# Kernel tuning notes

Hardware: AMD Instinct MI355X
Metric: run time of the kernel (lower is better)

Reference implementation:

```python
import jax, jax.numpy as jnp
import numpy as np

N = 100_000   # nodes
E = 3_200_000 # directed edges (avg degree 32)
D = 256       # feature dim (in_channels)
K = 2         # k of k-MIS


def _propagate_min(min_rank, row, col, n, k):
    # k iterations of scatter_min along edges (row -> col), keeping current value
    for _ in range(k):
        neigh = jax.ops.segment_min(min_rank[row], col, num_segments=n)
        min_rank = jnp.minimum(min_rank, neigh)
    return min_rank


def maximal_k_independent_set(row, col, rank, n, k):
    # Luby-style greedy k-MIS: repeatedly add nodes whose rank is minimal in their
    # k-hop in-neighbourhood, then mark (cover) the k-hop neighbourhood of the MIS.
    def dilate(mask):
        for _ in range(k):
            neigh = jax.ops.segment_max(mask[row].astype(jnp.int32), col, num_segments=n)
            mask = mask | (neigh > 0)
        return mask

    def cond(state):
        _, mask, _ = state
        return ~jnp.all(mask)

    def body(state):
        mis, mask, min_rank = state
        min_rank = _propagate_min(min_rank, row, col, n, k)
        mis = mis | (rank == min_rank)
        mask = dilate(mis)
        min_rank = jnp.where(mask, n, rank)  # covered nodes get rank 'infinity' (= n)
        return mis, mask, min_rank

    z = jnp.zeros((n,), dtype=bool)
    mis, _, _ = jax.lax.while_loop(cond, body, (z, z, rank))
    return mis


def cluster_k_mis(mis, row, col, rank, n, k):
    # min_rank = n everywhere except MIS nodes get their rank; propagate min k hops;
    # cluster id = index of the unique MIS rank each node ends up attached to.
    min_rank = jnp.where(mis, rank, n)
    min_rank = _propagate_min(min_rank, row, col, n, k)
    _, clusters = jnp.unique(min_rank, return_inverse=True)
    return clusters.reshape(-1).astype(jnp.int32)


def setup_inputs():
    key = jax.random.key(0)
    k1, k2, k3 = jax.random.split(key, 3)
    x = jax.random.normal(k1, (N, D), dtype=jnp.float32)
    edge_index = jax.random.randint(k2, (2, E), 0, N, dtype=jnp.int32)
    edge_attr = jax.random.normal(k3, (E,), dtype=jnp.float32)
    return {"x": x, "edge_index": edge_index, "edge_attr": edge_attr}


def reference(x, edge_index, edge_attr):
    n = x.shape[0]
    row, col = edge_index[0], edge_index[1]
    # scorer=None -> score = arange(n); greedy ordering of arange -> rank = arange(n)
    rank = jnp.arange(n, dtype=jnp.int32)

    mis = maximal_k_independent_set(row, col, rank, n, K)
    cluster = cluster_k_mis(mis, row, col, rank, n, K)
    c = int(mis.sum())  # number of clusters (MIS size)

    # --- pooled adjacency: coalesce duplicate (cluster[row], cluster[col]) with sum ---
    cl_np = np.asarray(cluster).astype(np.int64)
    r = cl_np[np.asarray(row)]
    cc = cl_np[np.asarray(col)]
    keys = r * np.int64(c) + cc
    uniq, inv = np.unique(keys, return_inverse=True)
    val = jax.ops.segment_sum(edge_attr, jnp.asarray(inv.astype(np.int32)),
                              num_segments=int(uniq.shape[0]))
    new_row = (uniq // c).astype(np.int32)
    new_col = (uniq % c).astype(np.int32)
    keep = np.nonzero(new_row != new_col)[0]  # remove_self_loops=True
    pooled_edge_index = jnp.stack([jnp.asarray(new_row[keep]), jnp.asarray(new_col[keep])])
    pooled_edge_attr = val[jnp.asarray(keep)]

    # --- pooled node features: reduce_x='sum' (adaptive=False, so no score scaling) ---
    x_pooled = jax.ops.segment_sum(x, cluster, num_segments=c)
    return x_pooled, pooled_edge_index, pooled_edge_attr
```

## Files before the change

### kernel.cpp

```cpp
#include <hip/hip_runtime.h>
#include <cmath>
#include <cstdint>

#define NT 256
#define EG0 1024
#define EG1 256
#define MAX_ROUND 16
#define SCAN_T 32
#define SCAN_IPB (NT*SCAN_T)
#define SENT 0x80000000u


__device__ __forceinline__ int block_append(int* cursor, bool pred, int* s_w){
  int wid  = threadIdx.x >> 6;
  int lane = threadIdx.x & 63;
  unsigned long long m = __ballot(pred);
  int cnt = __popcll(m);
  if(lane==0) s_w[wid]=cnt;
  __syncthreads();
  if(threadIdx.x==0){
    int t0=s_w[0], t1=s_w[1], t2=s_w[2], t3=s_w[3];
    int tot=t0+t1+t2+t3;
    int base = tot ? atomicAdd(cursor, tot) : 0;
    s_w[0]=base; s_w[1]=base+t0; s_w[2]=base+t0+t1; s_w[3]=base+t0+t1+t2;
  }
  __syncthreads();
  int pos = s_w[wid] + __popcll(m & ((1ull<<lane)-1ull));
  __syncthreads();
  return pos;
}


__global__ void k_init(int* a, int* b, int n){
  int v = blockIdx.x*NT + threadIdx.x;
  if(v<n){ a[v]=v; b[v]=v; }
}

__global__ void k_fill_dense(float* dense, long M){
  long stride = (long)gridDim.x*NT;
  for(long i = (long)blockIdx.x*NT + threadIdx.x; i<M; i+=stride)
    ((unsigned int*)dense)[i] = SENT;
}


__global__ void k_hop0(int* b, const int* __restrict__ row,
                       const int* __restrict__ col, int E){
  int stride = gridDim.x*NT;
  for(int e = blockIdx.x*NT + threadIdx.x; e<E; e+=stride){
    int s = row[e];
    if(s < b[col[e]]) atomicMin(&b[col[e]], s);
  }
}

__global__ void k_hop0f(int* a, const int* b, const int* __restrict__ row,
                        const int* __restrict__ col, int n, int E){
  int stride = gridDim.x*NT;
  int total = n + E;
  for(int i = blockIdx.x*NT + threadIdx.x; i<total; i+=stride){
    if(i<n){
      if(b[i] < a[i]) atomicMin(&a[i], b[i]);
    } else {
      int e = i-n;
      int s = b[row[e]];
      if(s < a[col[e]]) atomicMin(&a[col[e]], s);
    }
  }
}

__global__ void k_dil0(const int* a, int* d2, int* cover, const int* __restrict__ row,
                       const int* __restrict__ col, int E, int ep){
  int stride = gridDim.x*NT;
  for(int e = blockIdx.x*NT + threadIdx.x; e<E; e+=stride){
    int r = row[e];
    if(a[r]==r){
      int cc = col[e];
      d2[r]=ep;  cover[r]=1;
      d2[cc]=ep; cover[cc]=1;
    }
  }
}

__global__ void k_dil20(const int* a, const int* d2, int* cover, const int* __restrict__ row,
                        const int* __restrict__ col, int E, int ep){
  int stride = gridDim.x*NT;
  for(int e = blockIdx.x*NT + threadIdx.x; e<E; e+=stride){
    int r = row[e];
    if((d2[r]==ep || a[r]==r) && !cover[col[e]]) cover[col[e]]=1;
  }
}

__global__ void k_fincomp0(int* a, int* b, int* mis, int* cover, int n,
                           const int* __restrict__ row, const int* __restrict__ col, int E,
                           int2* Ld, int* lcnt1, int* U1, int* rcnt0){
  __shared__ int s_w[4];
  long nth = (long)gridDim.x*NT;
  for(long base = (long)blockIdx.x*NT; base < n; base += nth){
    int v = (int)base + threadIdx.x;
    bool unc = false;
    if(v<n){
      int nw = (a[v]==v);
      if(nw){ mis[v]=1; if(!cover[v]) cover[v]=1; }
      int cov = cover[v] | nw;
      int val = cov ? n : v;
      a[v]=val; b[v]=val;
      unc = !cov;
    }
    int pos = block_append(rcnt0, unc, s_w);
    if(unc) U1[pos]=v;
  }
  for(long base = (long)blockIdx.x*NT; base < E; base += nth){
    int e = (int)base + threadIdx.x;
    bool keep=false; int2 ed;
    if(e<E){
      ed = make_int2(row[e], col[e]);
      keep = (!cover[ed.x]) || (!cover[ed.y]);
    }
    int pos = block_append(lcnt1, keep, s_w);
    if(keep) Ld[pos]=ed;
  }
}


__global__ void k_hop1(int* b, const int* a, const int2* L, const int* pE,
                       const int* gate){
  if(*gate==0) return;
  int E = *pE;
  int stride = gridDim.x*NT;
  for(int e = blockIdx.x*NT + threadIdx.x; e<E; e+=stride){
    int2 ed = L[e];
    int s = a[ed.x];
    if(s < b[ed.y]) atomicMin(&b[ed.y], s);
  }
}

__global__ void k_hop1f(int* a, const int* b, const int2* L, const int* pE,
                        const int* U, const int* pU, const int* gate){
  if(*gate==0) return;
  int E = *pE, un = *pU;
  int total = un + E;
  int stride = gridDim.x*NT;
  for(int i = blockIdx.x*NT + threadIdx.x; i<total; i+=stride){
    if(i<un){
      int u = U[i];
      if(b[u] < a[u]) atomicMin(&a[u], b[u]);
    } else {
      int2 ed = L[i-un];
      int s = b[ed.x];
      if(s < a[ed.y]) atomicMin(&a[ed.y], s);
    }
  }
}

__global__ void k_dil11(const int* a, int* d2, int* cover, int* mis, const int2* L,
                        const int* pE, const int* U, const int* pU, const int* gate, int ep){
  if(*gate==0) return;
  int E = *pE, un = *pU;
  int total = un + E;
  int stride = gridDim.x*NT;
  for(int i = blockIdx.x*NT + threadIdx.x; i<total; i+=stride){
    if(i<un){
      int u = U[i];
      if(a[u]==u){ mis[u]=1; cover[u]=1; d2[u]=ep; }
    } else {
      int2 ed = L[i-un];
      if(a[ed.x]==ed.x){ d2[ed.x]=ep; cover[ed.x]=1; d2[ed.y]=ep; cover[ed.y]=1; }
    }
  }
}

__global__ void k_dil21(const int* a, const int* d2, int* cover, const int2* L,
                        const int* pE, const int* gate, int ep){
  if(*gate==0) return;
  int E = *pE;
  int stride = gridDim.x*NT;
  for(int e = blockIdx.x*NT + threadIdx.x; e<E; e+=stride){
    int2 ed = L[e];
    if((d2[ed.x]==ep || a[ed.x]==ed.x) && !cover[ed.y]) cover[ed.y]=1;
  }
}

__global__ void k_fincomp1(int* a, int* b, const int* cover, int n,
                           const int2* Ls, const int* pE, int2* Ld, int* lcntD,
                           const int* Us, const int* pU, int* Ud, int* rcntD,
                           const int* gate){
  if(*gate==0) return;
  __shared__ int s_w[4];
  int E = *pE, un = *pU;
  long nth = (long)gridDim.x*NT;
  for(long base = (long)blockIdx.x*NT; base < un; base += nth){
    int i = (int)base + threadIdx.x;
    bool unc=false; int u=0;
    if(i<un){ u = Us[i]; unc = !cover[u]; }
    int pos = block_append(rcntD, unc, s_w);
    if(unc) Ud[pos]=u;
  }
  for(long base = (long)blockIdx.x*NT; base < E; base += nth){
    int e = (int)base + threadIdx.x;
    bool keep=false; int2 ed;
    if(e<E){
      ed = Ls[e];
      int vx = cover[ed.x] ? n : ed.x;  a[ed.x]=vx; b[ed.x]=vx;
      int vy = cover[ed.y] ? n : ed.y;  a[ed.y]=vy; b[ed.y]=vy;
      keep = (!cover[ed.x]) || (!cover[ed.y]);
    }
    int pos = block_append(lcntD, keep, s_w);
    if(keep) Ld[pos]=ed;
  }
}


__global__ void k_cluster_init(const int* mis, int* a, int* b, int n){
  int v = blockIdx.x*NT + threadIdx.x;
  if(v<n){ int m = mis[v] ? v : n; a[v]=m; b[v]=m; }
}

__global__ void k_chop1(int* b, const int* a, const int* __restrict__ row,
                        const int* __restrict__ col, int n, int E){
  int stride = gridDim.x*NT;
  for(int e = blockIdx.x*NT + threadIdx.x; e<E; e+=stride){
    int s = a[row[e]];
    if(s < n && s < b[col[e]]) atomicMin(&b[col[e]], s);
  }
}

__global__ void k_chop2f(int* a, const int* b, const int* __restrict__ row,
                         const int* __restrict__ col, int n, int E){
  int stride = gridDim.x*NT;
  int total = n + E;
  for(int i = blockIdx.x*NT + threadIdx.x; i<total; i+=stride){
    if(i<n){
      if(b[i] < a[i]) atomicMin(&a[i], b[i]);
    } else {
      int e = i-n;
      int s = b[row[e]];
      if(s < n && s < a[col[e]]) atomicMin(&a[col[e]], s);
    }
  }
}

__global__ void k_mark(const int* mr, const int* mis, int* present, int* cmis, int n){
  int v = blockIdx.x*NT + threadIdx.x;
  int m = 0;
  if(v<n){
    int r = mr[v];
    if(r<n) present[r]=1;
    m = mis[v];
  }
  __shared__ int sh[NT];
  sh[threadIdx.x]=m; __syncthreads();
  for(int off=NT/2; off>0; off>>=1){
    if(threadIdx.x<off) sh[threadIdx.x]+=sh[threadIdx.x+off];
    __syncthreads();
  }
  if(threadIdx.x==0 && sh[0]) atomicAdd(cmis, sh[0]);
}


__global__ void k_scan1(const int* A, int M, int* bsum){
  int t = threadIdx.x;
  long base = (long)blockIdx.x*SCAN_IPB + (long)t*SCAN_T;
  int s = 0;
  #pragma unroll
  for(int j=0;j<SCAN_T;j++){ long i=base+j; if(i<M) s += A[i]; }
  __shared__ int sh[NT];
  sh[t]=s; __syncthreads();
  for(int off=NT/2; off>0; off>>=1){ if(t<off) sh[t]+=sh[t+off]; __syncthreads(); }
  if(t==0) bsum[blockIdx.x]=sh[0];
}

__global__ void k_scan2(const int* bsum, int* bscan, int B, int* totalOut){
  __shared__ int sh[NT];
  int t = threadIdx.x;
  int carry = 0;
  for(int base=0; base<B; base+=NT){
    int i = base+t;
    int v = (i<B) ? bsum[i] : 0;
    sh[t]=v; __syncthreads();
    for(int off=1; off<NT; off<<=1){
      int x=0; if(t>=off) x=sh[t-off];
      __syncthreads();
      sh[t]+=x; __syncthreads();
    }
    int incl = sh[t];
    if(i<B) bscan[i] = carry + incl - v;
    carry += sh[NT-1];
    __syncthreads();
  }
  if(t==0 && totalOut) *totalOut = carry;
}

__global__ void k_scan3(const int* A, int M, const int* bscan, int* pref){
  int t = threadIdx.x;
  long base = (long)blockIdx.x*SCAN_IPB + (long)t*SCAN_T;
  int s = 0;
  #pragma unroll
  for(int j=0;j<SCAN_T;j++){ long i=base+j; if(i<M) s += A[i]; }
  __shared__ int sh[NT];
  sh[t]=s; __syncthreads();
  for(int off=1; off<NT; off<<=1){
    int x=0; if(t>=off) x=sh[t-off];
    __syncthreads();
    sh[t]+=x; __syncthreads();
  }
  int run = bscan[blockIdx.x] + (sh[t]-s);
  for(int j=0;j<SCAN_T;j++){
    long i=base+j;
    if(i<M){ pref[i]=run; run += A[i]; }
  }
}


__global__ void k_assign(const int* mr, const int* pref, int* cl, int* ccount, int n){
  int v = blockIdx.x*NT + threadIdx.x;
  if(v<n){
    int r = mr[v];
    int cid = (r<n) ? pref[r] : 0;
    cl[v]=cid;
    atomicAdd(&ccount[cid],1);
  }
}

__global__ void k_scatter_nodes(const int* cl, const int* cstart, int* cursor, int* nodeList, int n){
  int v = blockIdx.x*NT + threadIdx.x;
  if(v<n){
    int cid = cl[v];
    int pos = cstart[cid] + atomicAdd(&cursor[cid],1);
    nodeList[pos]=v;
  }
}

__global__ void k_pool_x(const float* __restrict__ x, const int* nodeList, const int* cstart,
                         const int* ccount, const int* scal, float* out, long out_size){
  int c = scal[0], U = scal[1];
  int t = threadIdx.x;
  for(int cid=blockIdx.x; cid<c; cid+=gridDim.x){
    float s0=0.f, s1=0.f, s2=0.f, s3=0.f;
    if(cid<U){
      int st = cstart[cid], cn = ccount[cid];
      int i=0;
      for(; i+3<cn; i+=4){
        int n0=nodeList[st+i], n1=nodeList[st+i+1], n2=nodeList[st+i+2], n3=nodeList[st+i+3];
        s0 += x[(size_t)n0*256 + t];
        s1 += x[(size_t)n1*256 + t];
        s2 += x[(size_t)n2*256 + t];
        s3 += x[(size_t)n3*256 + t];
      }
      for(; i<cn; i++) s0 += x[(size_t)nodeList[st+i]*256 + t];
      s0 += s1+s2+s3;
    }
    long idx = (long)cid*256 + t;
    if(idx < out_size) out[idx]=s0;
  }
}

__global__ void k_edge_pool(const int* __restrict__ row, const int* __restrict__ col,
                            const float* __restrict__ attr, const int* cl,
                            const int* scal, float* dense, int E, long CMsq){
  int c = scal[0];
  int stride = gridDim.x*NT;
  for(int e = blockIdx.x*NT + threadIdx.x; e<E; e+=stride){
    long key = (long)cl[row[e]]*c + cl[col[e]];
    if(key < CMsq){
      unsafeAtomicAdd(&dense[key], attr[e]);
    }
  }
}

__device__ __forceinline__ int cellp(const float* dense, long i){
  return __float_as_uint(dense[i]) != SENT;
}

__global__ void k_cscan1(const float* dense, const int* scal, int* bsum, long CMsq){
  int c = scal[0];
  long M = (long)c*c; if(M>CMsq) M=CMsq;
  int t = threadIdx.x;
  long base = (long)blockIdx.x*SCAN_IPB + (long)t*SCAN_T;
  int s = 0;
  if(base < M && c > 0){
    int r = (int)(base / c);
    int q = (int)(base - (long)r*c);
    for(int j=0;j<SCAN_T;j++){
      long i=base+j;
      if(i<M){
        if(cellp(dense,i) && r!=q) s++;
      }
      if(++q==c){ q=0; r++; }
    }
  }
  __shared__ int sh[NT];
  sh[t]=s; __syncthreads();
  for(int off=NT/2; off>0; off>>=1){ if(t<off) sh[t]+=sh[t+off]; __syncthreads(); }
  if(t==0) bsum[blockIdx.x]=sh[0];
}

__global__ void k_cemit(const float* dense, const int* scal,
                        const int* bscan, float* out, long out_size, long CMsq){
  int c = scal[0]; int P = scal[2];
  long M = (long)c*c; if(M>CMsq) M=CMsq;
  long xoff = (long)c*256;
  int t = threadIdx.x;
  long base = (long)blockIdx.x*SCAN_IPB + (long)t*SCAN_T;
  int s = 0;
  int r0=0,q0=0;
  if(base < M && c > 0){
    r0 = (int)(base / c);
    q0 = (int)(base - (long)r0*c);
    int r=r0, q=q0;
    for(int j=0;j<SCAN_T;j++){
      long i=base+j;
      if(i<M){
        if(cellp(dense,i) && r!=q) s++;
      }
      if(++q==c){ q=0; r++; }
    }
  }
  __shared__ int sh[NT];
  sh[t]=s; __syncthreads();
  for(int off=1; off<NT; off<<=1){
    int x=0; if(t>=off) x=sh[t-off];
    __syncthreads();
    sh[t]+=x; __syncthreads();
  }
  int run = bscan[blockIdx.x] + (sh[t]-s);
  if(base < M && c > 0){
    int r=r0, q=q0;
    for(int j=0;j<SCAN_T;j++){
      long i=base+j;
      if(i<M && cellp(dense,i) && r!=q){
        long o0 = xoff + run;
        long o1 = xoff + (long)P + run;
        long o2 = xoff + 2L*(long)P + run;
        if(o0<out_size) out[o0]=(float)r;
        if(o1<out_size) out[o1]=(float)q;
        if(o2<out_size) out[o2]=dense[i];
        run++;
      }
      if(++q==c){ q=0; r++; }
    }
  }
}


extern "C" void kernel_launch(void* const* d_in, const int* in_sizes, int n_in,
                              void* d_out, int out_size, void* d_ws, size_t ws_size,
                              hipStream_t stream){
  (void)n_in;
  const float* x     = (const float*)d_in[0];
  const int*   eidx  = (const int*)d_in[1];
  const float* eattr = (const float*)d_in[2];
  const int D = 256;
  int n = in_sizes[0]/D;
  int E = in_sizes[1]/2;
  const int* row = eidx;
  const int* col = eidx + E;

  char* p = (char*)d_ws;
  auto alloc = [&](size_t bytes)->char*{ char* r=p; p += (bytes+255)&~(size_t)255; return r; };
  int2* LA   = (int2*)alloc((size_t)E*8);
  int2* LB   = (int2*)alloc((size_t)E*8);
  int* a     = (int*)alloc((size_t)n*4);
  int* b     = (int*)alloc((size_t)n*4);
  int* cl    = (int*)alloc((size_t)n*4);
  int* nodeList = (int*)alloc((size_t)n*4);
  int* pref  = (int*)alloc((size_t)n*4);
  int* U1    = (int*)alloc((size_t)n*4);
  int* U2    = (int*)alloc((size_t)n*4);
  int* bsum  = (int*)alloc(4096*4);
  int* bscan = (int*)alloc(4096*4);
  char* zstart = p;
  int* mis     = (int*)alloc((size_t)n*4);
  int* cover   = (int*)alloc((size_t)n*4);
  int* d2      = (int*)alloc((size_t)n*4);
  int* present = (int*)alloc((size_t)n*4);
  int* ccount  = (int*)alloc((size_t)n*4);
  int* cursor  = (int*)alloc((size_t)n*4);
  int* rcnt    = (int*)alloc((MAX_ROUND+2)*4);
  int* lcnt    = (int*)alloc((MAX_ROUND+2)*4);
  int* scal    = (int*)alloc(64);
  size_t zbytes = (size_t)(p - zstart);

  size_t used   = (size_t)(p-(char*)d_ws);
  size_t remain = (ws_size > used+4096) ? ws_size-used-4096 : 0;
  size_t cells  = remain/4;
  long CM = (long)std::sqrt((double)cells);
  while(CM>1 && CM*CM > (long)cells) CM--;
  if(CM>4096) CM=4096;
  if(CM<1) CM=1;
  long CMsq = CM*CM;
  float* dense = (float*)alloc((size_t)CMsq*4);

  hipMemsetAsync(zstart, 0, zbytes, stream);
  k_fill_dense<<<2048,NT,0,stream>>>(dense, CMsq);

  int NB  = (n+NT-1)/NT;
  int NBs = (n+SCAN_IPB-1)/SCAN_IPB;
  int CB  = (int)((CMsq+SCAN_IPB-1)/SCAN_IPB);

  k_init    <<<NB,NT,0,stream>>>(a,b,n);
  k_hop0    <<<EG0,NT,0,stream>>>(b,row,col,E);
  k_hop0f   <<<EG0,NT,0,stream>>>(a,b,row,col,n,E);
  k_dil0    <<<EG0,NT,0,stream>>>(a,d2,cover,row,col,E,1);
  k_dil20   <<<EG0,NT,0,stream>>>(a,d2,cover,row,col,E,1);
  k_fincomp0<<<EG0,NT,0,stream>>>(a,b,mis,cover,n,row,col,E,LB,&lcnt[1],U1,&rcnt[0]);

  for(int r=1; r<MAX_ROUND; ++r){
    int2* Ls = (r&1) ? LB : LA;
    int2* Ld = (r&1) ? LA : LB;
    int*  Us = (r&1) ? U1 : U2;
    int*  Ud = (r&1) ? U2 : U1;
    int ep = r+1;
    k_hop1    <<<EG1,NT,0,stream>>>(b,a,Ls,&lcnt[r],&rcnt[r-1]);
    k_hop1f   <<<EG1,NT,0,stream>>>(a,b,Ls,&lcnt[r],Us,&rcnt[r-1],&rcnt[r-1]);
    k_dil11   <<<EG1,NT,0,stream>>>(a,d2,cover,mis,Ls,&lcnt[r],Us,&rcnt[r-1],&rcnt[r-1],ep);
    k_dil21   <<<EG1,NT,0,stream>>>(a,d2,cover,Ls,&lcnt[r],&rcnt[r-1],ep);
    k_fincomp1<<<EG1,NT,0,stream>>>(a,b,cover,n,Ls,&lcnt[r],Ld,&lcnt[r+1],
                                    Us,&rcnt[r-1],Ud,&rcnt[r],&rcnt[r-1]);
  }

  k_cluster_init<<<NB,NT,0,stream>>>(mis,a,b,n);
  k_chop1 <<<EG0,NT,0,stream>>>(b,a,row,col,n,E);
  k_chop2f<<<EG0,NT,0,stream>>>(a,b,row,col,n,E);

  k_mark <<<NB,NT,0,stream>>>(a,mis,present,scal,n);
  k_scan1<<<NBs,NT,0,stream>>>(present,n,bsum);
  k_scan2<<<1,NT,0,stream>>>(bsum,bscan,NBs,scal+1);
  k_scan3<<<NBs,NT,0,stream>>>(present,n,bscan,pref);
  k_assign<<<NB,NT,0,stream>>>(a,pref,cl,ccount,n);

  k_scan1<<<NBs,NT,0,stream>>>(ccount,n,bsum);
  k_scan2<<<1,NT,0,stream>>>(bsum,bscan,NBs,nullptr);
  k_scan3<<<NBs,NT,0,stream>>>(ccount,n,bscan,pref);
  k_scatter_nodes<<<NB,NT,0,stream>>>(cl,pref,cursor,nodeList,n);

  k_pool_x<<<1024,NT,0,stream>>>(x,nodeList,pref,ccount,scal,(float*)d_out,(long)out_size);

  k_edge_pool<<<EG0,NT,0,stream>>>(row,col,eattr,cl,scal,dense,E,CMsq);
  k_cscan1<<<CB,NT,0,stream>>>(dense,scal,bsum,CMsq);
  k_scan2 <<<1,NT,0,stream>>>(bsum,bscan,CB,scal+2);
  k_cemit <<<CB,NT,0,stream>>>(dense,scal,bscan,(float*)d_out,(long)out_size,CMsq);
}
```

Baseline: 1.914 ms.

## Use MIS bitmaps, prune cluster propagation, size dense fill by cluster count

Replaces the int MIS array with a bitmap and adds a reach-1 bitmap, so the cluster min-propagation only does atomic work on edges whose source is an MIS node or was reached in hop one. The dense adjacency fill now runs after the cluster count is known and clears only c*c cells instead of the whole buffer. The ccount scan is limited to the number of output clusters, and pooled feature summation uses 1024-thread blocks that split each cluster's nodes across four groups and reduce them in shared memory. Together these cut memory traffic and wasted work, at the cost of extra bitmap atomics and more syncs in pool_x.

```diff
diff --git a/kernel.cpp b/kernel.cpp
--- a/kernel.cpp
+++ b/kernel.cpp
@@ -10,6 +10,14 @@
 #define SCAN_IPB (NT*SCAN_T)
 #define SENT 0x80000000u
 
+
+__device__ __forceinline__ int getbit(const unsigned int* bm, int v){
+  return (bm[v>>5]>>(v&31))&1u;
+}
+__device__ __forceinline__ void setbit(unsigned int* bm, int v){
+  unsigned int m = 1u<<(v&31);
+  if(!(bm[v>>5]&m)) atomicOr(&bm[v>>5], m);
+}
 
 __device__ __forceinline__ int block_append(int* cursor, bool pred, int* s_w){
   int wid  = threadIdx.x >> 6;
@@ -36,7 +44,9 @@
   if(v<n){ a[v]=v; b[v]=v; }
 }
 
-__global__ void k_fill_dense(float* dense, long M){
+__global__ void k_fill_dense(float* dense, const int* scal, long CMsq){
+  long c = scal[0];
+  long M = c*c; if(M>CMsq) M=CMsq;
   long stride = (long)gridDim.x*NT;
   for(long i = (long)blockIdx.x*NT + threadIdx.x; i<M; i+=stride)
     ((unsigned int*)dense)[i] = SENT;
@@ -89,7 +99,7 @@
   }
 }
 
-__global__ void k_fincomp0(int* a, int* b, int* mis, int* cover, int n,
+__global__ void k_fincomp0(int* a, int* b, unsigned int* misb, int* cover, int n,
                            const int* __restrict__ row, const int* __restrict__ col, int E,
                            int2* Ld, int* lcnt1, int* U1, int* rcnt0){
   __shared__ int s_w[4];
@@ -99,7 +109,7 @@
     bool unc = false;
     if(v<n){
       int nw = (a[v]==v);
-      if(nw){ mis[v]=1; if(!cover[v]) cover[v]=1; }
+      if(nw){ setbit(misb,v); if(!cover[v]) cover[v]=1; }
       int cov = cover[v] | nw;
       int val = cov ? n : v;
       a[v]=val; b[v]=val;
@@ -151,8 +161,9 @@
   }
 }
 
-__global__ void k_dil11(const int* a, int* d2, int* cover, int* mis, const int2* L,
-                        const int* pE, const int* U, const int* pU, const int* gate, int ep){
+__global__ void k_dil11(const int* a, int* d2, int* cover, unsigned int* misb,
+                        const int2* L, const int* pE, const int* U, const int* pU,
+                        const int* gate, int ep){
   if(*gate==0) return;
   int E = *pE, un = *pU;
   int total = un + E;
@@ -160,7 +171,7 @@
   for(int i = blockIdx.x*NT + threadIdx.x; i<total; i+=stride){
     if(i<un){
       int u = U[i];
-      if(a[u]==u){ mis[u]=1; cover[u]=1; d2[u]=ep; }
+      if(a[u]==u){ setbit(misb,u); cover[u]=1; d2[u]=ep; }
     } else {
       int2 ed = L[i-un];
       if(a[ed.x]==ed.x){ d2[ed.x]=ep; cover[ed.x]=1; d2[ed.y]=ep; cover[ed.y]=1; }
@@ -209,22 +220,33 @@
 }
 
 
-__global__ void k_cluster_init(const int* mis, int* a, int* b, int n){
+__global__ void k_cluster_init(const unsigned int* misb, unsigned int* reach1b,
+                               int* a, int* b, int n){
   int v = blockIdx.x*NT + threadIdx.x;
-  if(v<n){ int m = mis[v] ? v : n; a[v]=m; b[v]=m; }
-}
-
-__global__ void k_chop1(int* b, const int* a, const int* __restrict__ row,
-                        const int* __restrict__ col, int n, int E){
-  int stride = gridDim.x*NT;
-  for(int e = blockIdx.x*NT + threadIdx.x; e<E; e+=stride){
-    int s = a[row[e]];
-    if(s < n && s < b[col[e]]) atomicMin(&b[col[e]], s);
-  }
-}
-
-__global__ void k_chop2f(int* a, const int* b, const int* __restrict__ row,
-                         const int* __restrict__ col, int n, int E){
+  if(v<n){
+    int m = getbit(misb,v);
+    int val = m ? v : n;
+    a[v]=val; b[v]=val;
+    if(m) setbit(reach1b,v);
+  }
+}
+
+__global__ void k_chop1(int* b, const unsigned int* misb, unsigned int* reach1b,
+                        const int* __restrict__ row, const int* __restrict__ col, int E){
+  int stride = gridDim.x*NT;
+  for(int e = blockIdx.x*NT + threadIdx.x; e<E; e+=stride){
+    int r = row[e];
+    if(getbit(misb,r)){
+      int cc = col[e];
+      if(r < b[cc]) atomicMin(&b[cc], r);
+      setbit(reach1b, cc);
+    }
+  }
+}
+
+__global__ void k_chop2f(int* a, const int* b, const unsigned int* reach1b,
+                         const int* __restrict__ row, const int* __restrict__ col,
+                         int n, int E){
   int stride = gridDim.x*NT;
   int total = n + E;
   for(int i = blockIdx.x*NT + threadIdx.x; i<total; i+=stride){
@@ -232,19 +254,22 @@
       if(b[i] < a[i]) atomicMin(&a[i], b[i]);
     } else {
       int e = i-n;
-      int s = b[row[e]];
-      if(s < n && s < a[col[e]]) atomicMin(&a[col[e]], s);
-    }
-  }
-}
-
-__global__ void k_mark(const int* mr, const int* mis, int* present, int* cmis, int n){
+      int r = row[e];
+      if(getbit(reach1b,r)){
+        int s = b[r];
+        if(s < n && s < a[col[e]]) atomicMin(&a[col[e]], s);
+      }
+    }
+  }
+}
+
+__global__ void k_mark(const int* mr, const unsigned int* misb, int* present, int* cmis, int n){
   int v = blockIdx.x*NT + threadIdx.x;
   int m = 0;
   if(v<n){
     int r = mr[v];
-    if(r<n) present[r]=1;
-    m = mis[v];
+    if(r<n && !present[r]) present[r]=1;
+    m = getbit(misb,v);
   }
   __shared__ int sh[NT];
   sh[threadIdx.x]=m; __syncthreads();
@@ -329,27 +354,27 @@
   }
 }
 
-__global__ void k_pool_x(const float* __restrict__ x, const int* nodeList, const int* cstart,
-                         const int* ccount, const int* scal, float* out, long out_size){
+__global__ void __launch_bounds__(1024)
+k_pool_x(const float* __restrict__ x, const int* nodeList, const int* cstart,
+         const int* ccount, const int* scal, float* out, long out_size){
+  __shared__ float sh[4][256];
   int c = scal[0], U = scal[1];
-  int t = threadIdx.x;
+  int t = threadIdx.x & 255;
+  int g = threadIdx.x >> 8;
   for(int cid=blockIdx.x; cid<c; cid+=gridDim.x){
-    float s0=0.f, s1=0.f, s2=0.f, s3=0.f;
+    float s = 0.f;
     if(cid<U){
       int st = cstart[cid], cn = ccount[cid];
-      int i=0;
-      for(; i+3<cn; i+=4){
-        int n0=nodeList[st+i], n1=nodeList[st+i+1], n2=nodeList[st+i+2], n3=nodeList[st+i+3];
-        s0 += x[(size_t)n0*256 + t];
-        s1 += x[(size_t)n1*256 + t];
-        s2 += x[(size_t)n2*256 + t];
-        s3 += x[(size_t)n3*256 + t];
-      }
-      for(; i<cn; i++) s0 += x[(size_t)nodeList[st+i]*256 + t];
-      s0 += s1+s2+s3;
-    }
-    long idx = (long)cid*256 + t;
-    if(idx < out_size) out[idx]=s0;
+      for(int i=g; i<cn; i+=4)
+        s += x[(size_t)nodeList[st+i]*256 + t];
+    }
+    sh[g][t]=s;
+    __syncthreads();
+    if(g==0){
+      long idx = (long)cid*256 + t;
+      if(idx < out_size) out[idx] = sh[0][t]+sh[1][t]+sh[2][t]+sh[3][t];
+    }
+    __syncthreads();
   }
 }
 
@@ -453,6 +478,8 @@
   int E = in_sizes[1]/2;
   const int* row = eidx;
   const int* col = eidx + E;
+  int nwords = (n+31)>>5;
+  int CU_B = out_size/256 + 1; if(CU_B > n) CU_B = n;
 
   char* p = (char*)d_ws;
   auto alloc = [&](size_t bytes)->char*{ char* r=p; p += (bytes+255)&~(size_t)255; return r; };
@@ -468,9 +495,10 @@
   int* bsum  = (int*)alloc(4096*4);
   int* bscan = (int*)alloc(4096*4);
   char* zstart = p;
-  int* mis     = (int*)alloc((size_t)n*4);
   int* cover   = (int*)alloc((size_t)n*4);
   int* d2      = (int*)alloc((size_t)n*4);
+  unsigned int* misb    = (unsigned int*)alloc((size_t)nwords*4);
+  unsigned int* reach1b = (unsigned int*)alloc((size_t)nwords*4);
   int* present = (int*)alloc((size_t)n*4);
   int* ccount  = (int*)alloc((size_t)n*4);
   int* cursor  = (int*)alloc((size_t)n*4);
@@ -490,10 +518,10 @@
   float* dense = (float*)alloc((size_t)CMsq*4);
 
   hipMemsetAsync(zstart, 0, zbytes, stream);
-  k_fill_dense<<<2048,NT,0,stream>>>(dense, CMsq);
 
   int NB  = (n+NT-1)/NT;
   int NBs = (n+SCAN_IPB-1)/SCAN_IPB;
+  int NBc = (CU_B+SCAN_IPB-1)/SCAN_IPB;
   int CB  = (int)((CMsq+SCAN_IPB-1)/SCAN_IPB);
 
   k_init    <<<NB,NT,0,stream>>>(a,b,n);
@@ -501,7 +529,7 @@
   k_hop0f   <<<EG0,NT,0,stream>>>(a,b,row,col,n,E);
   k_dil0    <<<EG0,NT,0,stream>>>(a,d2,cover,row,col,E,1);
   k_dil20   <<<EG0,NT,0,stream>>>(a,d2,cover,row,col,E,1);
-  k_fincomp0<<<EG0,NT,0,stream>>>(a,b,mis,cover,n,row,col,E,LB,&lcnt[1],U1,&rcnt[0]);
+  k_fincomp0<<<EG0,NT,0,stream>>>(a,b,misb,cover,n,row,col,E,LB,&lcnt[1],U1,&rcnt[0]);
 
   for(int r=1; r<MAX_ROUND; ++r){
     int2* Ls = (r&1) ? LB : LA;
@@ -511,28 +539,30 @@
     int ep = r+1;
     k_hop1    <<<EG1,NT,0,stream>>>(b,a,Ls,&lcnt[r],&rcnt[r-1]);
     k_hop1f   <<<EG1,NT,0,stream>>>(a,b,Ls,&lcnt[r],Us,&rcnt[r-1],&rcnt[r-1]);
-    k_dil11   <<<EG1,NT,0,stream>>>(a,d2,cover,mis,Ls,&lcnt[r],Us,&rcnt[r-1],&rcnt[r-1],ep);
+    k_dil11   <<<EG1,NT,0,stream>>>(a,d2,cover,misb,Ls,&lcnt[r],Us,&rcnt[r-1],&rcnt[r-1],ep);
     k_dil21   <<<EG1,NT,0,stream>>>(a,d2,cover,Ls,&lcnt[r],&rcnt[r-1],ep);
     k_fincomp1<<<EG1,NT,0,stream>>>(a,b,cover,n,Ls,&lcnt[r],Ld,&lcnt[r+1],
                                     Us,&rcnt[r-1],Ud,&rcnt[r],&rcnt[r-1]);
   }
 
-  k_cluster_init<<<NB,NT,0,stream>>>(mis,a,b,n);
-  k_chop1 <<<EG0,NT,0,stream>>>(b,a,row,col,n,E);
-  k_chop2f<<<EG0,NT,0,stream>>>(a,b,row,col,n,E);
-
-  k_mark <<<NB,NT,0,stream>>>(a,mis,present,scal,n);
+  k_cluster_init<<<NB,NT,0,stream>>>(misb,reach1b,a,b,n);
+  k_chop1 <<<EG0,NT,0,stream>>>(b,misb,reach1b,row,col,E);
+  k_chop2f<<<EG0,NT,0,stream>>>(a,b,reach1b,row,col,n,E);
+
+  k_mark <<<NB,NT,0,stream>>>(a,misb,present,scal,n);
   k_scan1<<<NBs,NT,0,stream>>>(present,n,bsum);
   k_scan2<<<1,NT,0,stream>>>(bsum,bscan,NBs,scal+1);
   k_scan3<<<NBs,NT,0,stream>>>(present,n,bscan,pref);
   k_assign<<<NB,NT,0,stream>>>(a,pref,cl,ccount,n);
 
-  k_scan1<<<NBs,NT,0,stream>>>(ccount,n,bsum);
-  k_scan2<<<1,NT,0,stream>>>(bsum,bscan,NBs,nullptr);
-  k_scan3<<<NBs,NT,0,stream>>>(ccount,n,bscan,pref);
+  k_fill_dense<<<2048,NT,0,stream>>>(dense,scal,CMsq);
+
+  k_scan1<<<NBc,NT,0,stream>>>(ccount,CU_B,bsum);
+  k_scan2<<<1,NT,0,stream>>>(bsum,bscan,NBc,nullptr);
+  k_scan3<<<NBc,NT,0,stream>>>(ccount,CU_B,bscan,pref);
   k_scatter_nodes<<<NB,NT,0,stream>>>(cl,pref,cursor,nodeList,n);
 
-  k_pool_x<<<1024,NT,0,stream>>>(x,nodeList,pref,ccount,scal,(float*)d_out,(long)out_size);
+  k_pool_x<<<1024,1024,0,stream>>>(x,nodeList,pref,ccount,scal,(float*)d_out,(long)out_size);
 
   k_edge_pool<<<EG0,NT,0,stream>>>(row,col,eattr,cl,scal,dense,E,CMsq);
   k_cscan1<<<CB,NT,0,stream>>>(dense,scal,bsum,CMsq);
```

Measured after the change: 1.933 ms. Within noise of the previous version (+1.0%).
